# Kernel optimization log

Hardware: AMD Instinct MI355X
Metric: run time of the kernel (lower is better)

## Reference

```python
import jax, jax.numpy as jnp
import numpy as np

N = 16384
IN_DIM = 512
EMBED_DIM = 256

def setup_inputs() -> dict:
    key = jax.random.key(0)
    k1, k2, k3 = jax.random.split(key, 3)
    adj = jax.random.uniform(k1, (N, N), dtype=jnp.float32)
    x = jax.random.normal(k2, (N, IN_DIM), dtype=jnp.float32)
    # nn.Linear default init scale ~ 1/sqrt(in_dim)
    W = jax.random.normal(k3, (EMBED_DIM, IN_DIM), dtype=jnp.float32) / np.sqrt(IN_DIM)
    return {"adj": adj, "x": x, "W": W}

def reference(adj, x, W):
    # laplace = diag(1/(rowsum(adj)+1) + 1); mm(laplace, x) == row-wise scale
    d = 1.0 / (jnp.sum(adj, axis=1) + 1.0) + 1.0          # [N]
    h = (d[:, None] * x) @ W.T                              # [N, EMBED_DIM]
    return jax.nn.relu(h)
```

## Files before the change

### kernel.cpp

```cpp
#include <hip/hip_runtime.h>
#include <hip/hip_bf16.h>

#define NROWS 16384
#define KDIM  512
#define EDIM  256
#define BM    64
#define BK    64

typedef __attribute__((ext_vector_type(8))) short  short8;
typedef __attribute__((ext_vector_type(4))) float  floatx4;
typedef __attribute__((ext_vector_type(4))) unsigned short ushort4_t;

static __device__ __forceinline__ unsigned short f2bf(float f) {
    union { float f; unsigned int u; } v; v.f = f;
    return (unsigned short)((v.u + 0x7FFFu + ((v.u >> 16) & 1u)) >> 16);
}

__global__ __launch_bounds__(512) void fused_kernel(const float* __restrict__ adj,
                                                    const float* __restrict__ x,
                                                    const float* __restrict__ W,
                                                    float* __restrict__ out) {
    __shared__ unsigned short As[BM * BK];
    __shared__ unsigned short Bs[EDIM * BK];
    __shared__ float dsc[BM];

    const int m0 = blockIdx.x * BM;
    const int t  = threadIdx.x;
    const int l  = t & 63;
    const int w  = t >> 6;

    {
        const floatx4* p = (const floatx4*)(adj + (size_t)(m0 + w * 8) * NROWS);
#pragma unroll
        for (int rr = 0; rr < 8; ++rr) {
            const floatx4* q = p + (size_t)rr * (NROWS / 4);
            float s0 = 0.f, s1 = 0.f, s2 = 0.f, s3 = 0.f;
#pragma unroll 4
            for (int i = 0; i < 64; i += 4) {
                floatx4 v0 = __builtin_nontemporal_load(&q[l + (i + 0) * 64]);
                floatx4 v1 = __builtin_nontemporal_load(&q[l + (i + 1) * 64]);
                floatx4 v2 = __builtin_nontemporal_load(&q[l + (i + 2) * 64]);
                floatx4 v3 = __builtin_nontemporal_load(&q[l + (i + 3) * 64]);
                s0 += (v0.x + v0.y) + (v0.z + v0.w);
                s1 += (v1.x + v1.y) + (v1.z + v1.w);
                s2 += (v2.x + v2.y) + (v2.z + v2.w);
                s3 += (v3.x + v3.y) + (v3.z + v3.w);
            }
            float s = (s0 + s1) + (s2 + s3);
#pragma unroll
            for (int off = 32; off > 0; off >>= 1)
                s += __shfl_down(s, off, 64);
            if (l == 0) dsc[w * 8 + rr] = 1.0f / (s + 1.0f) + 1.0f;
        }
    }

    const int lr = l & 15;
    const int lh = l >> 4;
    const int wm = w >> 2;
    const int wn = w & 3;

    floatx4 acc[2][4] = {};

    for (int k0 = 0; k0 < KDIM; k0 += BK) {
        if (k0) __syncthreads();

        {
            const int kq = (t & 15) * 4;
            int r = t >> 4;
#pragma unroll
            for (int p = 0; p < 2; ++p, r += 32) {
                float4 v = *(const float4*)(x + (size_t)(m0 + r) * KDIM + k0 + kq);
                ushort4_t o = { f2bf(v.x), f2bf(v.y), f2bf(v.z), f2bf(v.w) };
                const int idx = (r * BK + kq) ^ ((r & 7) << 3);
                *(ushort4_t*)&As[idx] = o;
            }
        }
        {
            const int kq = (t & 15) * 4;
            int n = t >> 4;
#pragma unroll
            for (int p = 0; p < 8; ++p, n += 32) {
                float4 v = *(const float4*)(W + (size_t)n * KDIM + k0 + kq);
                ushort4_t o = { f2bf(v.x), f2bf(v.y), f2bf(v.z), f2bf(v.w) };
                const int idx = (n * BK + kq) ^ ((n & 7) << 3);
                *(ushort4_t*)&Bs[idx] = o;
            }
        }
        __syncthreads();

#pragma unroll
        for (int kc = 0; kc < 2; ++kc) {
            const int kk = kc * 32 + lh * 8;
            short8 a[2], b[4];
#pragma unroll
            for (int mf = 0; mf < 2; ++mf) {
                const int r = wm * 32 + mf * 16 + lr;
                a[mf] = *(const short8*)&As[(r * BK + kk) ^ ((r & 7) << 3)];
            }
#pragma unroll
            for (int nf = 0; nf < 4; ++nf) {
                const int n = wn * 64 + nf * 16 + lr;
                b[nf] = *(const short8*)&Bs[(n * BK + kk) ^ ((n & 7) << 3)];
            }
#pragma unroll
            for (int mf = 0; mf < 2; ++mf)
#pragma unroll
                for (int nf = 0; nf < 4; ++nf)
                    acc[mf][nf] = __builtin_amdgcn_mfma_f32_16x16x32_bf16(
                        a[mf], b[nf], acc[mf][nf], 0, 0, 0);
        }
    }

#pragma unroll
    for (int mf = 0; mf < 2; ++mf) {
#pragma unroll
        for (int j = 0; j < 4; ++j) {
            const int rloc = wm * 32 + mf * 16 + lh * 4 + j;
            const float dscale = dsc[rloc];
            const size_t row = m0 + rloc;
#pragma unroll
            for (int nf = 0; nf < 4; ++nf) {
                const int col = wn * 64 + nf * 16 + lr;
                out[row * EDIM + col] = fmaxf(acc[mf][nf][j] * dscale, 0.f);
            }
        }
    }
}

extern "C" void kernel_launch(void* const* d_in, const int* in_sizes, int n_in,
                              void* d_out, int out_size, void* d_ws, size_t ws_size,
                              hipStream_t stream) {
    const float* adj = (const float*)d_in[0];
    const float* x   = (const float*)d_in[1];
    const float* W   = (const float*)d_in[2];
    float* out = (float*)d_out;

    fused_kernel<<<NROWS / BM, 512, 0, stream>>>(adj, x, W, out);
}
```

Baseline: 178.3 us.

## Halve row tile and alternate rowsum/GEMM phase order across block groups

Result: slower. 181.9 us (+2.0%).

```diff
diff --git a/kernel.cpp b/kernel.cpp
--- a/kernel.cpp
+++ b/kernel.cpp
@@ -4,7 +4,7 @@
 #define NROWS 16384
 #define KDIM  512
 #define EDIM  256
-#define BM    64
+#define BM    32
 #define BK    64
 
 typedef __attribute__((ext_vector_type(8))) short  short8;
@@ -16,10 +16,10 @@
     return (unsigned short)((v.u + 0x7FFFu + ((v.u >> 16) & 1u)) >> 16);
 }
 
-__global__ __launch_bounds__(512) void fused_kernel(const float* __restrict__ adj,
-                                                    const float* __restrict__ x,
-                                                    const float* __restrict__ W,
-                                                    float* __restrict__ out) {
+__global__ __launch_bounds__(512, 4) void fused_kernel(const float* __restrict__ adj,
+                                                       const float* __restrict__ x,
+                                                       const float* __restrict__ W,
+                                                       float* __restrict__ out) {
     __shared__ unsigned short As[BM * BK];
     __shared__ unsigned short Bs[EDIM * BK];
     __shared__ float dsc[BM];
@@ -28,11 +28,15 @@
     const int t  = threadIdx.x;
     const int l  = t & 63;
     const int w  = t >> 6;
+    const int lr = l & 15;
+    const int lh = l >> 4;
 
-    {
-        const floatx4* p = (const floatx4*)(adj + (size_t)(m0 + w * 8) * NROWS);
+    floatx4 acc[2][2] = {};
+
+    auto rowsum_phase = [&]() {
+        const floatx4* p = (const floatx4*)(adj + (size_t)(m0 + w * 4) * NROWS);
 #pragma unroll
-        for (int rr = 0; rr < 8; ++rr) {
+        for (int rr = 0; rr < 4; ++rr) {
             const floatx4* q = p + (size_t)rr * (NROWS / 4);
             float s0 = 0.f, s1 = 0.f, s2 = 0.f, s3 = 0.f;
 #pragma unroll 4
@@ -50,78 +54,81 @@
 #pragma unroll
             for (int off = 32; off > 0; off >>= 1)
                 s += __shfl_down(s, off, 64);
-            if (l == 0) dsc[w * 8 + rr] = 1.0f / (s + 1.0f) + 1.0f;
+            if (l == 0) dsc[w * 4 + rr] = 1.0f / (s + 1.0f) + 1.0f;
         }
-    }
+    };
 
-    const int lr = l & 15;
-    const int lh = l >> 4;
-    const int wm = w >> 2;
-    const int wn = w & 3;
+    auto gemm_phase = [&]() {
+        for (int k0 = 0; k0 < KDIM; k0 += BK) {
+            if (k0) __syncthreads();
 
-    floatx4 acc[2][4] = {};
-
-    for (int k0 = 0; k0 < KDIM; k0 += BK) {
-        if (k0) __syncthreads();
-
-        {
-            const int kq = (t & 15) * 4;
-            int r = t >> 4;
-#pragma unroll
-            for (int p = 0; p < 2; ++p, r += 32) {
-                float4 v = *(const float4*)(x + (size_t)(m0 + r) * KDIM + k0 + kq);
+            {
+                const int kq = (t & 15) * 4;
+                const int r  = t >> 4;
+                floatx4 v = __builtin_nontemporal_load(
+                    (const floatx4*)(x + (size_t)(m0 + r) * KDIM + k0 + kq));
                 ushort4_t o = { f2bf(v.x), f2bf(v.y), f2bf(v.z), f2bf(v.w) };
                 const int idx = (r * BK + kq) ^ ((r & 7) << 3);
                 *(ushort4_t*)&As[idx] = o;
             }
-        }
-        {
-            const int kq = (t & 15) * 4;
-            int n = t >> 4;
+            {
+                const int kq = (t & 15) * 4;
+                int n = t >> 4;
+#pragma unroll 2
+                for (int p = 0; p < 8; ++p, n += 32) {
+                    float4 v = *(const float4*)(W + (size_t)n * KDIM + k0 + kq);
+                    ushort4_t o = { f2bf(v.x), f2bf(v.y), f2bf(v.z), f2bf(v.w) };
+                    const int idx = (n * BK + kq) ^ ((n & 7) << 3);
+                    *(ushort4_t*)&Bs[idx] = o;
+                }
+            }
+            __syncthreads();
+
 #pragma unroll
-            for (int p = 0; p < 8; ++p, n += 32) {
-                float4 v = *(const float4*)(W + (size_t)n * KDIM + k0 + kq);
-                ushort4_t o = { f2bf(v.x), f2bf(v.y), f2bf(v.z), f2bf(v.w) };
-                const int idx = (n * BK + kq) ^ ((n & 7) << 3);
-                *(ushort4_t*)&Bs[idx] = o;
+            for (int kc = 0; kc < 2; ++kc) {
+                const int kk = kc * 32 + lh * 8;
+                short8 a[2], b[2];
+#pragma unroll
+                for (int mf = 0; mf < 2; ++mf) {
+                    const int r = mf * 16 + lr;
+                    a[mf] = *(const short8*)&As[(r * BK + kk) ^ ((r & 7) << 3)];
+                }
+#pragma unroll
+                for (int nf = 0; nf < 2; ++nf) {
+                    const int n = w * 32 + nf * 16 + lr;
+                    b[nf] = *(const short8*)&Bs[(n * BK + kk) ^ ((n & 7) << 3)];
+                }
+#pragma unroll
+                for (int mf = 0; mf < 2; ++mf)
+#pragma unroll
+                    for (int nf = 0; nf < 2; ++nf)
+                        acc[mf][nf] = __builtin_amdgcn_mfma_f32_16x16x32_bf16(
+                            a[mf], b[nf], acc[mf][nf], 0, 0, 0);
             }
         }
+    };
+
+    if ((blockIdx.x >> 8) & 1) {
+        gemm_phase();
+        rowsum_phase();
         __syncthreads();
-
-#pragma unroll
-        for (int kc = 0; kc < 2; ++kc) {
-            const int kk = kc * 32 + lh * 8;
-            short8 a[2], b[4];
-#pragma unroll
-            for (int mf = 0; mf < 2; ++mf) {
-                const int r = wm * 32 + mf * 16 + lr;
-                a[mf] = *(const short8*)&As[(r * BK + kk) ^ ((r & 7) << 3)];
-            }
-#pragma unroll
-            for (int nf = 0; nf < 4; ++nf) {
-                const int n = wn * 64 + nf * 16 + lr;
-                b[nf] = *(const short8*)&Bs[(n * BK + kk) ^ ((n & 7) << 3)];
-            }
-#pragma unroll
-            for (int mf = 0; mf < 2; ++mf)
-#pragma unroll
-                for (int nf = 0; nf < 4; ++nf)
-                    acc[mf][nf] = __builtin_amdgcn_mfma_f32_16x16x32_bf16(
-                        a[mf], b[nf], acc[mf][nf], 0, 0, 0);
-        }
+    } else {
+        rowsum_phase();
+        gemm_phase();
     }
 
 #pragma unroll
     for (int mf = 0; mf < 2; ++mf) {
 #pragma unroll
         for (int j = 0; j < 4; ++j) {
-            const int rloc = wm * 32 + mf * 16 + lh * 4 + j;
+            const int rloc = mf * 16 + lh * 4 + j;
             const float dscale = dsc[rloc];
             const size_t row = m0 + rloc;
 #pragma unroll
-            for (int nf = 0; nf < 4; ++nf) {
-                const int col = wn * 64 + nf * 16 + lr;
-                out[row * EDIM + col] = fmaxf(acc[mf][nf][j] * dscale, 0.f);
+            for (int nf = 0; nf < 2; ++nf) {
+                const int col = w * 32 + nf * 16 + lr;
+                __builtin_nontemporal_store(fmaxf(acc[mf][nf][j] * dscale, 0.f),
+                                            &out[row * EDIM + col]);
             }
         }
     }
```
